# Kernel tuning notes

Hardware: AMD Instinct MI355X
Metric: run time of the kernel (lower is better)

The kernel has to match this reference:

```python
import jax, jax.numpy as jnp
import numpy as np

STATE_LEN, SEQ_LEN, HIDDEN = 2048, 4096, 2048

def setup_inputs() -> dict:
    key = jax.random.key(0)
    k1, k2, k3, k4 = jax.random.split(key, 4)
    scale = 1.0 / np.sqrt(HIDDEN)
    return {
        "out_state": jax.random.normal(k1, (STATE_LEN, HIDDEN), dtype=jnp.float32),
        "history": jax.random.normal(k2, (SEQ_LEN, HIDDEN), dtype=jnp.float32),
        "W": jax.random.normal(k3, (HIDDEN, HIDDEN), dtype=jnp.float32) * scale,
        "b": jax.random.normal(k4, (HIDDEN,), dtype=jnp.float32) * scale,
    }

def reference(out_state, history, W, b):
    # method='general': energy_j = Linear(history_j) = history_j @ W.T + b
    # score[i, j] = out_state_i . energy_j  -> batched GEMM replacing the double loop
    energies = history @ W.T + b                 # [seq_len, hidden]
    scores = jnp.einsum('ih,jh->ij', out_state, energies)  # [state_len, seq_len]
    # F.softmax on a 2D tensor (legacy default) normalizes over dim=1 (rows)
    return jax.nn.softmax(scores, axis=-1)
```

## Files before the change

### kernel.cpp

```cpp
#include <hip/hip_runtime.h>


#define STATE_LEN 2048
#define SEQ_LEN   4096
#define HIDDEN    2048

#define BK 32

#define WAIT_VM8   0x0F78
#define WAIT_VM0   0x0F70
#define WAIT_LGKM0 0xC07F

typedef __bf16 bf16x8 __attribute__((ext_vector_type(8)));
typedef float f32x4 __attribute__((ext_vector_type(4)));

__device__ __forceinline__ unsigned short f32_to_bf16(float f) {
  unsigned u = __float_as_uint(f);
  u += 0x7FFFu + ((u >> 16) & 1u);
  return (unsigned short)(u >> 16);
}
__device__ __forceinline__ float bf16_to_f32(unsigned short h) {
  return __uint_as_float(((unsigned)h) << 16);
}

__device__ __forceinline__ void gld16(const void* g, void* l) {
  __builtin_amdgcn_global_load_lds(
      (const __attribute__((address_space(1))) unsigned int*)g,
      (__attribute__((address_space(3))) unsigned int*)l,
      16, 0, 0);
}

__global__ __launch_bounds__(256) void pack_all(
    const float* __restrict__ os, const float* __restrict__ hist,
    const float* __restrict__ W,
    unsigned short* __restrict__ ohi, unsigned short* __restrict__ olo,
    unsigned short* __restrict__ hhi, unsigned short* __restrict__ hlo,
    unsigned short* __restrict__ wthi, unsigned short* __restrict__ wtlo) {
  const int bx = blockIdx.x;
  const int t = threadIdx.x;
  if (bx >= 1024) {
    const int b2 = bx - 1024;
    const float* in;
    unsigned short *hi, *lo;
    int i;
    if (b2 < 4096) {
      in = os; hi = ohi; lo = olo; i = (b2 * 256 + t) * 4;
    } else {
      in = hist; hi = hhi; lo = hlo; i = ((b2 - 4096) * 256 + t) * 4;
    }
    float4 v = *(const float4*)&in[i];
    ushort4 h, l;
    h.x = f32_to_bf16(v.x); l.x = f32_to_bf16(v.x - bf16_to_f32(h.x));
    h.y = f32_to_bf16(v.y); l.y = f32_to_bf16(v.y - bf16_to_f32(h.y));
    h.z = f32_to_bf16(v.z); l.z = f32_to_bf16(v.z - bf16_to_f32(h.z));
    h.w = f32_to_bf16(v.w); l.w = f32_to_bf16(v.w - bf16_to_f32(h.w));
    *(ushort4*)&hi[i] = h;
    *(ushort4*)&lo[i] = l;
  } else {
    __shared__ float tile[64][65];
    const int bt = bx;
    const int h0 = (bt & 31) * 64;
    const int k0 = (bt >> 5) * 64;
    const int lr = t >> 4;
    const int c4 = (t & 15) * 4;
#pragma unroll
    for (int pass = 0; pass < 4; ++pass) {
      const int row = pass * 16 + lr;
      float4 v = *(const float4*)&W[(size_t)(h0 + row) * HIDDEN + k0 + c4];
      tile[row][c4] = v.x; tile[row][c4 + 1] = v.y;
      tile[row][c4 + 2] = v.z; tile[row][c4 + 3] = v.w;
    }
    __syncthreads();
#pragma unroll
    for (int pass = 0; pass < 4; ++pass) {
      const int kl = pass * 16 + (t >> 4);
      const int hl = (t & 15) * 4;
      ushort4 h4, l4;
#pragma unroll
      for (int j = 0; j < 4; ++j) {
        const float x = tile[hl + j][kl];
        const unsigned short h = f32_to_bf16(x);
        ((unsigned short*)&h4)[j] = h;
        ((unsigned short*)&l4)[j] = f32_to_bf16(x - bf16_to_f32(h));
      }
      const size_t o = (size_t)(k0 + kl) * HIDDEN + h0 + hl;
      *(ushort4*)&wthi[o] = h4;
      *(ushort4*)&wtlo[o] = l4;
    }
  }
}

__global__ __launch_bounds__(256) void reduce_split4(
    const float* __restrict__ p0, const float* __restrict__ p1,
    const float* __restrict__ p2, const float* __restrict__ p3,
    unsigned short* __restrict__ hi, unsigned short* __restrict__ lo, int n) {
  int i = (blockIdx.x * 256 + threadIdx.x) * 4;
  if (i >= n) return;
  float4 a = *(const float4*)&p0[i];
  float4 b = *(const float4*)&p1[i];
  float4 c = *(const float4*)&p2[i];
  float4 d = *(const float4*)&p3[i];
  a.x = (a.x + b.x) + (c.x + d.x);
  a.y = (a.y + b.y) + (c.y + d.y);
  a.z = (a.z + b.z) + (c.z + d.z);
  a.w = (a.w + b.w) + (c.w + d.w);
  ushort4 h, l;
  h.x = f32_to_bf16(a.x); l.x = f32_to_bf16(a.x - bf16_to_f32(h.x));
  h.y = f32_to_bf16(a.y); l.y = f32_to_bf16(a.y - bf16_to_f32(h.y));
  h.z = f32_to_bf16(a.z); l.z = f32_to_bf16(a.z - bf16_to_f32(h.z));
  h.w = f32_to_bf16(a.w); l.w = f32_to_bf16(a.w - bf16_to_f32(h.w));
  *(ushort4*)&hi[i] = h;
  *(ushort4*)&lo[i] = l;
}

template <int KSPLIT>
__global__ __launch_bounds__(512, 2) void gemm_big(
    const unsigned short* __restrict__ Ahi, const unsigned short* __restrict__ Alo,
    const unsigned short* __restrict__ Bhi, const unsigned short* __restrict__ Blo,
    float* __restrict__ P0, float* __restrict__ P1,
    float* __restrict__ P2, float* __restrict__ P3,
    int M, int N, int K) {
  __shared__ __align__(16) unsigned short sA[2][2][256 * BK];
  __shared__ __align__(16) unsigned short sB[2][2][256 * BK];

  const int t = threadIdx.x;
  const int tileM = blockIdx.y * 256;
  const int tileN = blockIdx.x * 256;
  const int z = (KSPLIT > 1) ? blockIdx.z : 0;
  const int kBase = z * (K / KSPLIT);
  const int iters = (K / KSPLIT) / BK;
  float* Cf = (z == 0) ? P0 : (z == 1) ? P1 : (z == 2) ? P2 : P3;

  const int rr = t >> 2;
  const int cc = t & 3;

  const int lane = t & 63;
  const int wave = t >> 6;
  const int wm = wave >> 1;
  const int wn = wave & 1;
  const int lr = lane & 15;
  const int kqc = lane >> 4;

  f32x4 acc[4][8] = {};

  auto stage = [&](int buf, int k0) {
#pragma unroll
    for (int p = 0; p < 2; ++p) {
      const int r = p * 128 + rr;
      const int q = cc ^ ((r >> 1) & 3);
      const size_t ga = (size_t)(tileM + r) * K + k0 + q * 8;
      const size_t gb = (size_t)(tileN + r) * K + k0 + q * 8;
      const int ls = r * BK + cc * 8;
      gld16(Ahi + ga, &sA[buf][0][ls]);
      gld16(Alo + ga, &sA[buf][1][ls]);
      gld16(Bhi + gb, &sB[buf][0][ls]);
      gld16(Blo + gb, &sB[buf][1][ls]);
    }
  };

  stage(0, kBase);

  for (int it = 0; it < iters; ++it) {
    const int buf = it & 1;
    if (it + 1 < iters) {
      stage(buf ^ 1, kBase + (it + 1) * BK);
      __builtin_amdgcn_s_waitcnt(WAIT_VM8);
    } else {
      __builtin_amdgcn_s_waitcnt(WAIT_VM0);
    }
    __builtin_amdgcn_s_barrier();

    bf16x8 ah[4], al[4];
#pragma unroll
    for (int mi = 0; mi < 4; ++mi) {
      const int R = wm * 64 + mi * 16 + lr;
      const int off = R * BK + (kqc ^ ((R >> 1) & 3)) * 8;
      ah[mi] = *(const bf16x8*)&sA[buf][0][off];
      al[mi] = *(const bf16x8*)&sA[buf][1][off];
    }
#pragma unroll
    for (int nh = 0; nh < 2; ++nh) {
      bf16x8 bh[4], bl[4];
#pragma unroll
      for (int nj = 0; nj < 4; ++nj) {
        const int R = wn * 128 + (nh * 4 + nj) * 16 + lr;
        const int off = R * BK + (kqc ^ ((R >> 1) & 3)) * 8;
        bh[nj] = *(const bf16x8*)&sB[buf][0][off];
        bl[nj] = *(const bf16x8*)&sB[buf][1][off];
      }
#pragma unroll
      for (int mi = 0; mi < 4; ++mi)
#pragma unroll
        for (int nj = 0; nj < 4; ++nj) {
          f32x4 a = acc[mi][nh * 4 + nj];
          a = __builtin_amdgcn_mfma_f32_16x16x32_bf16(ah[mi], bh[nj], a, 0, 0, 0);
          a = __builtin_amdgcn_mfma_f32_16x16x32_bf16(ah[mi], bl[nj], a, 0, 0, 0);
          a = __builtin_amdgcn_mfma_f32_16x16x32_bf16(al[mi], bh[nj], a, 0, 0, 0);
          acc[mi][nh * 4 + nj] = a;
        }
    }

    __builtin_amdgcn_s_waitcnt(WAIT_LGKM0);
    __builtin_amdgcn_s_barrier();
  }

#pragma unroll
  for (int mi = 0; mi < 4; ++mi)
#pragma unroll
    for (int ni = 0; ni < 8; ++ni)
#pragma unroll
      for (int e = 0; e < 4; ++e) {
        const int row = tileM + wm * 64 + mi * 16 + (lane >> 4) * 4 + e;
        const int col = tileN + wn * 128 + ni * 16 + lr;
        Cf[(size_t)row * N + col] = acc[mi][ni][e];
      }
}

__global__ __launch_bounds__(256) void softmax_rows2(
    float* __restrict__ d, const float* __restrict__ p1, int cols) {
  const int row = blockIdx.x;
  float* p = d + (size_t)row * cols;
  const float* q = p1 + (size_t)row * cols;
  const int t = threadIdx.x;
  const int lane = t & 63;
  const int wave = t >> 6;
  __shared__ float sred[4];

  float4 v[4];
  float m = -3.0e38f;
#pragma unroll
  for (int k = 0; k < 4; ++k) {
    float4 a = *(const float4*)&p[(t + k * 256) * 4];
    float4 b = *(const float4*)&q[(t + k * 256) * 4];
    a.x += b.x; a.y += b.y; a.z += b.z; a.w += b.w;
    v[k] = a;
    m = fmaxf(m, fmaxf(fmaxf(a.x, a.y), fmaxf(a.z, a.w)));
  }
#pragma unroll
  for (int off = 32; off > 0; off >>= 1) m = fmaxf(m, __shfl_xor(m, off, 64));
  if (lane == 0) sred[wave] = m;
  __syncthreads();
  m = fmaxf(fmaxf(sred[0], sred[1]), fmaxf(sred[2], sred[3]));
  __syncthreads();

  float s = 0.f;
#pragma unroll
  for (int k = 0; k < 4; ++k) {
    v[k].x = __expf(v[k].x - m);
    v[k].y = __expf(v[k].y - m);
    v[k].z = __expf(v[k].z - m);
    v[k].w = __expf(v[k].w - m);
    s += (v[k].x + v[k].y) + (v[k].z + v[k].w);
  }
#pragma unroll
  for (int off = 32; off > 0; off >>= 1) s += __shfl_xor(s, off, 64);
  if (lane == 0) sred[wave] = s;
  __syncthreads();
  s = (sred[0] + sred[1]) + (sred[2] + sred[3]);
  const float inv = 1.0f / s;
#pragma unroll
  for (int k = 0; k < 4; ++k) {
    v[k].x *= inv; v[k].y *= inv; v[k].z *= inv; v[k].w *= inv;
    *(float4*)&p[(t + k * 256) * 4] = v[k];
  }
}

extern "C" void kernel_launch(void* const* d_in, const int* in_sizes, int n_in,
                              void* d_out, int out_size, void* d_ws, size_t ws_size,
                              hipStream_t stream) {
  const float* out_state = (const float*)d_in[0];
  const float* history   = (const float*)d_in[1];
  const float* W         = (const float*)d_in[2];
  float* out = (float*)d_out;

  char* ws = (char*)d_ws;
  const size_t MB = 1ull << 20;
  unsigned short* ohi  = (unsigned short*)(ws + 0 * MB);
  unsigned short* olo  = (unsigned short*)(ws + 8 * MB);
  unsigned short* wthi = (unsigned short*)(ws + 16 * MB);
  unsigned short* wtlo = (unsigned short*)(ws + 24 * MB);
  unsigned short* hhi  = (unsigned short*)(ws + 32 * MB);
  unsigned short* hlo  = (unsigned short*)(ws + 48 * MB);
  float*          pws  = (float*)(ws + 64 * MB);

  const size_t QSZ = (size_t)STATE_LEN * HIDDEN;
  float* g1p0 = pws;
  float* g1p1 = pws + QSZ;
  float* g1p2 = out;
  float* g1p3 = out + QSZ;
  unsigned short* thi = (unsigned short*)(ws + 0 * MB);
  unsigned short* tlo = (unsigned short*)(ws + 8 * MB);

  pack_all<<<13312, 256, 0, stream>>>(out_state, history, W, ohi, olo, hhi, hlo,
                                      wthi, wtlo);
  gemm_big<4><<<dim3(HIDDEN / 256, STATE_LEN / 256, 4), 512, 0, stream>>>(
      ohi, olo, wthi, wtlo, g1p0, g1p1, g1p2, g1p3, STATE_LEN, HIDDEN, HIDDEN);
  reduce_split4<<<(STATE_LEN * HIDDEN) / 1024, 256, 0, stream>>>(
      g1p0, g1p1, g1p2, g1p3, thi, tlo, STATE_LEN * HIDDEN);
  gemm_big<2><<<dim3(SEQ_LEN / 256, STATE_LEN / 256, 2), 512, 0, stream>>>(
      thi, tlo, hhi, hlo, out, pws, nullptr, nullptr, STATE_LEN, SEQ_LEN, HIDDEN);
  softmax_rows2<<<STATE_LEN, 256, 0, stream>>>(out, pws, SEQ_LEN);
}
```

Baseline: 270.7 us.

## Split global prefetch into halves and interleave LDS loads with MFMA phases

Each prefetch stage is split into two halves so that half of the next tile's global-to-LDS loads is issued later, in the middle of the compute phase. The MFMA work is broken into four quadrant phases, separated by barriers and wrapped in s_setprio, in a ping-pong style schedule. The goal is to overlap memory issue with matrix math and let waves favour MFMA issue. The cost is several extra barriers per K-iteration and more live B registers, which could reduce occupancy or add stalls.

```diff
diff --git a/kernel.cpp b/kernel.cpp
--- a/kernel.cpp
+++ b/kernel.cpp
@@ -7,7 +7,7 @@
 
 #define BK 32
 
-#define WAIT_VM8   0x0F78
+#define WAIT_VM4   0x0F74
 #define WAIT_VM0   0x0F70
 #define WAIT_LGKM0 0xC07F
 
@@ -143,63 +143,84 @@
 
   f32x4 acc[4][8] = {};
 
-  auto stage = [&](int buf, int k0) {
-#pragma unroll
-    for (int p = 0; p < 2; ++p) {
-      const int r = p * 128 + rr;
-      const int q = cc ^ ((r >> 1) & 3);
-      const size_t ga = (size_t)(tileM + r) * K + k0 + q * 8;
-      const size_t gb = (size_t)(tileN + r) * K + k0 + q * 8;
-      const int ls = r * BK + cc * 8;
-      gld16(Ahi + ga, &sA[buf][0][ls]);
-      gld16(Alo + ga, &sA[buf][1][ls]);
-      gld16(Bhi + gb, &sB[buf][0][ls]);
-      gld16(Blo + gb, &sB[buf][1][ls]);
-    }
+  auto stage_half = [&](int buf, int k0, int p) {
+    const int r = p * 128 + rr;
+    const int q = cc ^ ((r >> 1) & 3);
+    const size_t ga = (size_t)(tileM + r) * K + k0 + q * 8;
+    const size_t gb = (size_t)(tileN + r) * K + k0 + q * 8;
+    const int ls = r * BK + cc * 8;
+    gld16(Ahi + ga, &sA[buf][0][ls]);
+    gld16(Alo + ga, &sA[buf][1][ls]);
+    gld16(Bhi + gb, &sB[buf][0][ls]);
+    gld16(Blo + gb, &sB[buf][1][ls]);
   };
 
-  stage(0, kBase);
+  stage_half(0, kBase, 0);
+  stage_half(0, kBase, 1);
 
   for (int it = 0; it < iters; ++it) {
     const int buf = it & 1;
+    const int k1 = kBase + (it + 1) * BK;
+
     if (it + 1 < iters) {
-      stage(buf ^ 1, kBase + (it + 1) * BK);
-      __builtin_amdgcn_s_waitcnt(WAIT_VM8);
+      stage_half(buf ^ 1, k1, 0);
+      __builtin_amdgcn_s_waitcnt(WAIT_VM4);
     } else {
       __builtin_amdgcn_s_waitcnt(WAIT_VM0);
     }
     __builtin_amdgcn_s_barrier();
 
-    bf16x8 ah[4], al[4];
-#pragma unroll
-    for (int mi = 0; mi < 4; ++mi) {
+    bf16x8 ah[4], al[4], bh[8], bl[8];
+    auto loadA = [&](int mi) {
       const int R = wm * 64 + mi * 16 + lr;
       const int off = R * BK + (kqc ^ ((R >> 1) & 3)) * 8;
       ah[mi] = *(const bf16x8*)&sA[buf][0][off];
       al[mi] = *(const bf16x8*)&sA[buf][1][off];
-    }
-#pragma unroll
-    for (int nh = 0; nh < 2; ++nh) {
-      bf16x8 bh[4], bl[4];
-#pragma unroll
-      for (int nj = 0; nj < 4; ++nj) {
-        const int R = wn * 128 + (nh * 4 + nj) * 16 + lr;
-        const int off = R * BK + (kqc ^ ((R >> 1) & 3)) * 8;
-        bh[nj] = *(const bf16x8*)&sB[buf][0][off];
-        bl[nj] = *(const bf16x8*)&sB[buf][1][off];
-      }
-#pragma unroll
-      for (int mi = 0; mi < 4; ++mi)
-#pragma unroll
-        for (int nj = 0; nj < 4; ++nj) {
-          f32x4 a = acc[mi][nh * 4 + nj];
+    };
+    auto loadB = [&](int nj) {
+      const int R = wn * 128 + nj * 16 + lr;
+      const int off = R * BK + (kqc ^ ((R >> 1) & 3)) * 8;
+      bh[nj] = *(const bf16x8*)&sB[buf][0][off];
+      bl[nj] = *(const bf16x8*)&sB[buf][1][off];
+    };
+    auto mfma_quad = [&](int mi0, int nj0) {
+#pragma unroll
+      for (int mi = mi0; mi < mi0 + 2; ++mi)
+#pragma unroll
+        for (int nj = nj0; nj < nj0 + 4; ++nj) {
+          f32x4 a = acc[mi][nj];
           a = __builtin_amdgcn_mfma_f32_16x16x32_bf16(ah[mi], bh[nj], a, 0, 0, 0);
           a = __builtin_amdgcn_mfma_f32_16x16x32_bf16(ah[mi], bl[nj], a, 0, 0, 0);
           a = __builtin_amdgcn_mfma_f32_16x16x32_bf16(al[mi], bh[nj], a, 0, 0, 0);
-          acc[mi][nh * 4 + nj] = a;
+          acc[mi][nj] = a;
         }
-    }
-
+    };
+
+    loadA(0); loadA(1);
+    loadB(0); loadB(1); loadB(2); loadB(3);
+    if (it + 1 < iters) stage_half(buf ^ 1, k1, 1);
+    loadA(2); loadA(3);
+    __builtin_amdgcn_s_barrier();
+
+    __builtin_amdgcn_s_setprio(1);
+    mfma_quad(0, 0);
+    __builtin_amdgcn_s_setprio(0);
+    __builtin_amdgcn_s_barrier();
+
+    loadB(4); loadB(5); loadB(6); loadB(7);
+    __builtin_amdgcn_s_setprio(1);
+    mfma_quad(2, 0);
+    __builtin_amdgcn_s_setprio(0);
+    __builtin_amdgcn_s_barrier();
+
+    __builtin_amdgcn_s_setprio(1);
+    mfma_quad(0, 4);
+    __builtin_amdgcn_s_setprio(0);
+    __builtin_amdgcn_s_barrier();
+
+    __builtin_amdgcn_s_setprio(1);
+    mfma_quad(2, 4);
+    __builtin_amdgcn_s_setprio(0);
     __builtin_amdgcn_s_waitcnt(WAIT_LGKM0);
     __builtin_amdgcn_s_barrier();
   }
```

Result: slower. 298.4 us (+10.2%).

## Switch GEMM to 32x32x16 MFMA tiles with XCD-aware block remap

Applied to the files above, without the earlier changes.

Replaces the 16x16x32 bf16 MFMA tiling with 32x32x16 MFMA, reorganising LDS fragment loads, accumulators and the epilogue store mapping. B fragments are now double-buffered in registers so the next column's loads overlap the current MFMAs. Block indices are also remapped so consecutive tiles land on the same XCD, which should improve L2 reuse. The larger MFMA shape cuts LDS read traffic per flop, at some risk of register pressure and a less coalesced epilogue.

```diff
diff --git a/kernel.cpp b/kernel.cpp
--- a/kernel.cpp
+++ b/kernel.cpp
@@ -13,6 +13,7 @@
 
 typedef __bf16 bf16x8 __attribute__((ext_vector_type(8)));
 typedef float f32x4 __attribute__((ext_vector_type(4)));
+typedef float f32x16 __attribute__((ext_vector_type(16)));
 
 __device__ __forceinline__ unsigned short f32_to_bf16(float f) {
   unsigned u = __float_as_uint(f);
@@ -124,9 +125,21 @@
   __shared__ __align__(16) unsigned short sB[2][2][256 * BK];
 
   const int t = threadIdx.x;
-  const int tileM = blockIdx.y * 256;
-  const int tileN = blockIdx.x * 256;
-  const int z = (KSPLIT > 1) ? blockIdx.z : 0;
+
+  const int gx = gridDim.x, gy = gridDim.y;
+  {
+  }
+  int flat = blockIdx.x + gx * (blockIdx.y + gy * blockIdx.z);
+  const int cpx = (gx * gy * gridDim.z) >> 3;
+  flat = (flat & 7) * cpx + (flat >> 3);
+  const int nbx = flat % gx;
+  const int tq  = flat / gx;
+  const int nby = tq % gy;
+  const int nbz = tq / gy;
+
+  const int tileM = nby * 256;
+  const int tileN = nbx * 256;
+  const int z = (KSPLIT > 1) ? nbz : 0;
   const int kBase = z * (K / KSPLIT);
   const int iters = (K / KSPLIT) / BK;
   float* Cf = (z == 0) ? P0 : (z == 1) ? P1 : (z == 2) ? P2 : P3;
@@ -138,10 +151,10 @@
   const int wave = t >> 6;
   const int wm = wave >> 1;
   const int wn = wave & 1;
-  const int lr = lane & 15;
-  const int kqc = lane >> 4;
-
-  f32x4 acc[4][8] = {};
+  const int l31 = lane & 31;
+  const int khalf = lane >> 5;
+
+  f32x16 acc[2][4] = {};
 
   auto stage = [&](int buf, int k0) {
 #pragma unroll
@@ -162,6 +175,7 @@
 
   for (int it = 0; it < iters; ++it) {
     const int buf = it & 1;
+
     if (it + 1 < iters) {
       stage(buf ^ 1, kBase + (it + 1) * BK);
       __builtin_amdgcn_s_waitcnt(WAIT_VM8);
@@ -170,33 +184,45 @@
     }
     __builtin_amdgcn_s_barrier();
 
-    bf16x8 ah[4], al[4];
-#pragma unroll
-    for (int mi = 0; mi < 4; ++mi) {
-      const int R = wm * 64 + mi * 16 + lr;
-      const int off = R * BK + (kqc ^ ((R >> 1) & 3)) * 8;
-      ah[mi] = *(const bf16x8*)&sA[buf][0][off];
-      al[mi] = *(const bf16x8*)&sA[buf][1][off];
-    }
-#pragma unroll
-    for (int nh = 0; nh < 2; ++nh) {
-      bf16x8 bh[4], bl[4];
-#pragma unroll
-      for (int nj = 0; nj < 4; ++nj) {
-        const int R = wn * 128 + (nh * 4 + nj) * 16 + lr;
-        const int off = R * BK + (kqc ^ ((R >> 1) & 3)) * 8;
-        bh[nj] = *(const bf16x8*)&sB[buf][0][off];
-        bl[nj] = *(const bf16x8*)&sB[buf][1][off];
+    bf16x8 ah[2][2], al[2][2];
+#pragma unroll
+    for (int mi = 0; mi < 2; ++mi) {
+      const int R = wm * 64 + mi * 32 + l31;
+      const int sw = (R >> 1) & 3;
+#pragma unroll
+      for (int ks = 0; ks < 2; ++ks) {
+        const int off = R * BK + ((ks * 2 + khalf) ^ sw) * 8;
+        ah[mi][ks] = *(const bf16x8*)&sA[buf][0][off];
+        al[mi][ks] = *(const bf16x8*)&sA[buf][1][off];
       }
-#pragma unroll
-      for (int mi = 0; mi < 4; ++mi)
-#pragma unroll
-        for (int nj = 0; nj < 4; ++nj) {
-          f32x4 a = acc[mi][nh * 4 + nj];
-          a = __builtin_amdgcn_mfma_f32_16x16x32_bf16(ah[mi], bh[nj], a, 0, 0, 0);
-          a = __builtin_amdgcn_mfma_f32_16x16x32_bf16(ah[mi], bl[nj], a, 0, 0, 0);
-          a = __builtin_amdgcn_mfma_f32_16x16x32_bf16(al[mi], bh[nj], a, 0, 0, 0);
-          acc[mi][nh * 4 + nj] = a;
+    }
+
+    bf16x8 bh[2][2], bl[2][2];
+    auto loadB = [&](int nj, int par) {
+      const int R = wn * 128 + nj * 32 + l31;
+      const int sw = (R >> 1) & 3;
+#pragma unroll
+      for (int ks = 0; ks < 2; ++ks) {
+        const int off = R * BK + ((ks * 2 + khalf) ^ sw) * 8;
+        bh[par][ks] = *(const bf16x8*)&sB[buf][0][off];
+        bl[par][ks] = *(const bf16x8*)&sB[buf][1][off];
+      }
+    };
+
+    loadB(0, 0);
+#pragma unroll
+    for (int nj = 0; nj < 4; ++nj) {
+      const int par = nj & 1;
+      if (nj < 3) loadB(nj + 1, par ^ 1);
+#pragma unroll
+      for (int mi = 0; mi < 2; ++mi)
+#pragma unroll
+        for (int ks = 0; ks < 2; ++ks) {
+          f32x16 a = acc[mi][nj];
+          a = __builtin_amdgcn_mfma_f32_32x32x16_bf16(ah[mi][ks], bh[par][ks], a, 0, 0, 0);
+          a = __builtin_amdgcn_mfma_f32_32x32x16_bf16(ah[mi][ks], bl[par][ks], a, 0, 0, 0);
+          a = __builtin_amdgcn_mfma_f32_32x32x16_bf16(al[mi][ks], bh[par][ks], a, 0, 0, 0);
+          acc[mi][nj] = a;
         }
     }
 
@@ -205,14 +231,14 @@
   }
 
 #pragma unroll
-  for (int mi = 0; mi < 4; ++mi)
-#pragma unroll
-    for (int ni = 0; ni < 8; ++ni)
-#pragma unroll
-      for (int e = 0; e < 4; ++e) {
-        const int row = tileM + wm * 64 + mi * 16 + (lane >> 4) * 4 + e;
-        const int col = tileN + wn * 128 + ni * 16 + lr;
-        Cf[(size_t)row * N + col] = acc[mi][ni][e];
+  for (int mi = 0; mi < 2; ++mi)
+#pragma unroll
+    for (int nj = 0; nj < 4; ++nj)
+#pragma unroll
+      for (int r = 0; r < 16; ++r) {
+        const int row = tileM + wm * 64 + mi * 32 + (r & 3) + 8 * (r >> 2) + 4 * khalf;
+        const int col = tileN + wn * 128 + nj * 32 + l31;
+        Cf[(size_t)row * N + col] = acc[mi][nj][r];
       }
 }
 
```

After: 285.6 us. +5.5%, slower.
